# Performance work log

Hardware: AMD Instinct MI355X
Metric: run time of the kernel (lower is better)

## Reference

```python
import jax, jax.numpy as jnp
import numpy as np

N = 50000       # nodes
E = 800000      # edges (avg degree 16)
IN_DIM = 128
H_DIM = 96      # conv='SKP' -> h_dim unchanged
OUT_DIM = 64
NUM_LAYERS = 4
HEADS = 2       # conv='SKP' -> num_heads forced to 2


def setup_inputs() -> dict:
    key = jax.random.key(0)
    ks = jax.random.split(key, 9)
    x = jax.random.normal(ks[0], (N, IN_DIM), jnp.float32)
    edge_index = jax.random.randint(ks[1], (2, E), 0, N, dtype=jnp.int32)
    enc_w = jax.random.normal(ks[2], (IN_DIM, H_DIM), jnp.float32) / np.sqrt(IN_DIM)
    enc_b = jnp.zeros((H_DIM,), jnp.float32)
    dec_w = jax.random.normal(ks[3], (H_DIM, OUT_DIM), jnp.float32) / np.sqrt(H_DIM)
    dec_b = jnp.zeros((OUT_DIM,), jnp.float32)
    # per-layer, per-head linear transforms of the SKP conv
    conv_W = jax.random.normal(ks[4], (NUM_LAYERS, HEADS, H_DIM, H_DIM), jnp.float32) / np.sqrt(H_DIM)
    # per-layer, per-head learnable edge weights (SKP takes num_edges at init)
    conv_ew = jax.random.normal(ks[5], (NUM_LAYERS, HEADS, E), jnp.float32) * 0.1
    return {"x": x, "edge_index": edge_index, "enc_w": enc_w, "enc_b": enc_b,
            "dec_w": dec_w, "dec_b": dec_b, "conv_W": conv_W, "conv_ew": conv_ew}


def _skp_conv(h, src, dst, W, ew):
    # h: [N, d], W: [H, d, d], ew: [H, E]
    # X' = sum_h S_h X W_h  (S_h = learned edge-weighted sparse propagation)
    m = jnp.einsum('nd,hde->hne', h, W)          # [H, N, d] per-head transform
    g = m[:, src, :]                              # [H, E, d] gather at source nodes
    comb = jnp.einsum('he,hed->ed', ew, g)        # weight per edge, sum heads -> [E, d]
    return jax.ops.segment_sum(comb, dst, num_segments=N)  # scatter-add to dest


def reference(x, edge_index, enc_w, enc_b, dec_w, dec_b, conv_W, conv_ew):
    src, dst = edge_index[0], edge_index[1]
    h = jax.nn.relu(x @ enc_w + enc_b)
    for l in range(NUM_LAYERS):
        h = _skp_conv(h, src, dst, conv_W[l], conv_ew[l])
        h = jax.nn.relu(h)   # act=True
    return (h @ dec_w + dec_b, h)
```

## Files before the change

kernel.cpp:

```cpp
#include <hip/hip_runtime.h>

constexpr int IND = 128;
constexpr int HD  = 96;
constexpr int OD  = 64;
constexpr int NL  = 4;

struct F3 { float x, y, z; };

__global__ __launch_bounds__(256) void k_hist(const int* __restrict__ dst, int* __restrict__ deg, int E) {
    int e = blockIdx.x * 256 + threadIdx.x;
    if (e < E) atomicAdd(&deg[dst[e]], 1);
}

__global__ __launch_bounds__(256) void k_scan1(const int* __restrict__ deg, int* __restrict__ bsum, int n) {
    int tid = threadIdx.x;
    int base = blockIdx.x * 1024 + tid * 4;
    int s = 0;
    #pragma unroll
    for (int q = 0; q < 4; ++q) { int i = base + q; if (i < n) s += deg[i]; }
    #pragma unroll
    for (int o = 32; o > 0; o >>= 1) s += __shfl_xor(s, o);
    __shared__ int wsum[4];
    int lane = tid & 63, wid = tid >> 6;
    if (lane == 0) wsum[wid] = s;
    __syncthreads();
    if (tid == 0) bsum[blockIdx.x] = wsum[0] + wsum[1] + wsum[2] + wsum[3];
}

__global__ void k_scan2(const int* __restrict__ bsum, int* __restrict__ boff, int nb,
                        int* __restrict__ row_ptr, int n, int E) {
    int l = threadIdx.x;
    int v = (l < nb) ? bsum[l] : 0;
    int incl = v;
    #pragma unroll
    for (int o = 1; o < 64; o <<= 1) { int t = __shfl_up(incl, o); if (l >= o) incl += t; }
    if (l < nb) boff[l] = incl - v;
    if (l == 0) row_ptr[n] = E;
}

__global__ __launch_bounds__(256) void k_scan3(const int* __restrict__ deg, const int* __restrict__ boff,
                                               int* __restrict__ row_ptr, int n) {
    int tid = threadIdx.x;
    int base = blockIdx.x * 1024 + tid * 4;
    int d[4];
    #pragma unroll
    for (int q = 0; q < 4; ++q) { int i = base + q; d[q] = (i < n) ? deg[i] : 0; }
    int tsum = d[0] + d[1] + d[2] + d[3];
    int incl = tsum;
    #pragma unroll
    for (int o = 1; o < 64; o <<= 1) { int t = __shfl_up(incl, o); if ((tid & 63) >= o) incl += t; }
    __shared__ int wsum[4];
    int lane = tid & 63, wid = tid >> 6;
    if (lane == 63) wsum[wid] = incl;
    __syncthreads();
    int woff = 0;
    for (int w = 0; w < wid; ++w) woff += wsum[w];
    int run = boff[blockIdx.x] + woff + (incl - tsum);
    #pragma unroll
    for (int q = 0; q < 4; ++q) {
        int i = base + q;
        if (i < n) { row_ptr[i] = run; run += d[q]; }
    }
}

__global__ __launch_bounds__(256) void k_fill(const int* __restrict__ src, const int* __restrict__ dst,
                                              const int* __restrict__ row_ptr, int* __restrict__ cursor,
                                              int2* __restrict__ sep, int E) {
    int e = blockIdx.x * 256 + threadIdx.x;
    if (e >= E) return;
    int d = dst[e];
    int pos = atomicAdd(&cursor[d], 1);
    sep[row_ptr[d] + pos] = make_int2(src[e], e);
}

__global__ __launch_bounds__(256) void k_perm2(const int2* __restrict__ sep,
                                               const float* __restrict__ cA0, const float* __restrict__ cA1,
                                               const float* __restrict__ cB0, const float* __restrict__ cB1,
                                               float2* __restrict__ ewq, int E) {
    int i = blockIdx.x * 256 + threadIdx.x;
    if (i >= E) return;
    int e = sep[i].y;
    ewq[i]     = make_float2(cA0[e], cA1[e]);
    ewq[E + i] = make_float2(cB0[e], cB1[e]);
}

__global__ __launch_bounds__(256) void k_agg(const float* __restrict__ h, const int* __restrict__ row_ptr,
                                             const int2* __restrict__ sep, const float2* __restrict__ ewq,
                                             float* __restrict__ A0, float* __restrict__ A1, int n) {
    int g = blockIdx.x * 8 + (threadIdx.x >> 5);
    int lane = threadIdx.x & 31;
    if (g >= n) return;
    int beg = row_ptr[g], end = row_ptr[g + 1];
    float a0x = 0.f, a0y = 0.f, a0z = 0.f;
    float a1x = 0.f, a1y = 0.f, a1z = 0.f;
    int off = lane * 3;
    int i = beg;
    for (; i + 4 <= end; i += 4) {
        int2 s0 = sep[i], s1 = sep[i + 1], s2 = sep[i + 2], s3 = sep[i + 3];
        float2 w0 = ewq[i], w1 = ewq[i + 1], w2 = ewq[i + 2], w3 = ewq[i + 3];
        F3 v0 = *(const F3*)(h + (size_t)s0.x * HD + off);
        F3 v1 = *(const F3*)(h + (size_t)s1.x * HD + off);
        F3 v2 = *(const F3*)(h + (size_t)s2.x * HD + off);
        F3 v3 = *(const F3*)(h + (size_t)s3.x * HD + off);
        a0x = fmaf(w0.x, v0.x, a0x); a0y = fmaf(w0.x, v0.y, a0y); a0z = fmaf(w0.x, v0.z, a0z);
        a1x = fmaf(w0.y, v0.x, a1x); a1y = fmaf(w0.y, v0.y, a1y); a1z = fmaf(w0.y, v0.z, a1z);
        a0x = fmaf(w1.x, v1.x, a0x); a0y = fmaf(w1.x, v1.y, a0y); a0z = fmaf(w1.x, v1.z, a0z);
        a1x = fmaf(w1.y, v1.x, a1x); a1y = fmaf(w1.y, v1.y, a1y); a1z = fmaf(w1.y, v1.z, a1z);
        a0x = fmaf(w2.x, v2.x, a0x); a0y = fmaf(w2.x, v2.y, a0y); a0z = fmaf(w2.x, v2.z, a0z);
        a1x = fmaf(w2.y, v2.x, a1x); a1y = fmaf(w2.y, v2.y, a1y); a1z = fmaf(w2.y, v2.z, a1z);
        a0x = fmaf(w3.x, v3.x, a0x); a0y = fmaf(w3.x, v3.y, a0y); a0z = fmaf(w3.x, v3.z, a0z);
        a1x = fmaf(w3.y, v3.x, a1x); a1y = fmaf(w3.y, v3.y, a1y); a1z = fmaf(w3.y, v3.z, a1z);
    }
    for (; i < end; ++i) {
        int2 s0 = sep[i];
        float2 w0 = ewq[i];
        F3 v0 = *(const F3*)(h + (size_t)s0.x * HD + off);
        a0x = fmaf(w0.x, v0.x, a0x); a0y = fmaf(w0.x, v0.y, a0y); a0z = fmaf(w0.x, v0.z, a0z);
        a1x = fmaf(w0.y, v0.x, a1x); a1y = fmaf(w0.y, v0.y, a1y); a1z = fmaf(w0.y, v0.z, a1z);
    }
    float* p0 = A0 + (size_t)g * HD + off;
    p0[0] = a0x; p0[1] = a0y; p0[2] = a0z;
    float* p1 = A1 + (size_t)g * HD + off;
    p1[0] = a1x; p1[1] = a1y; p1[2] = a1z;
}

template<int K, int NO, bool DUAL, bool RELU, bool BIAS>
__global__ __launch_bounds__(256) void k_gemm(const float* __restrict__ A0p, const float* __restrict__ A1p,
                                              const float* __restrict__ W0p,
                                              const float* __restrict__ bias,
                                              float* __restrict__ out, int n) {
    constexpr int BRO = 128;
    constexpr int KC  = K / 4;
    constexpr int NC  = NO / 16;
    __shared__ float sA[BRO * K];
    int tid = threadIdx.x;
    int tx = tid & 15;
    int ty = tid >> 4;
    int ty2 = ty & 3;
    int brow = blockIdx.x * BRO;

    float acc[8][NC];
    #pragma unroll
    for (int r = 0; r < 8; ++r)
        #pragma unroll
        for (int j = 0; j < NC; ++j) acc[r][j] = 0.f;

    #pragma unroll
    for (int head = 0; head < (DUAL ? 2 : 1); ++head) {
        if (head) __syncthreads();
        const float* Ah = head ? A1p : A0p;
        for (int j = tid; j < BRO * KC; j += 256) {
            int r = j / KC, c4 = j % KC;
            int gr = brow + r;
            float4 v = make_float4(0.f, 0.f, 0.f, 0.f);
            if (gr < n) v = *(const float4*)(Ah + (size_t)gr * K + 4 * c4);
            int sw = c4 ^ ((r >> 3) & 3);
            *(float4*)&sA[r * K + 4 * sw] = v;
        }
        __syncthreads();

        const float* Wh = W0p + (size_t)head * K * NO;
        #pragma unroll 2
        for (int kb4 = 0; kb4 < KC; ++kb4) {
            float4 a4[8];
            #pragma unroll
            for (int r = 0; r < 8; ++r)
                a4[r] = *(const float4*)&sA[(8 * ty + r) * K + 4 * (kb4 ^ ty2)];
            #pragma unroll
            for (int q = 0; q < 4; ++q) {
                float wv[NC];
                const float* wrow = Wh + (size_t)(4 * kb4 + q) * NO + NC * tx;
                #pragma unroll
                for (int j2 = 0; j2 < NC; j2 += 2) {
                    float2 w2 = *(const float2*)(wrow + j2);
                    wv[j2] = w2.x; wv[j2 + 1] = w2.y;
                }
                #pragma unroll
                for (int r = 0; r < 8; ++r) {
                    const float* ap = (const float*)&a4[r];
                    float av = ap[q];
                    #pragma unroll
                    for (int j2 = 0; j2 < NC; ++j2)
                        acc[r][j2] = fmaf(av, wv[j2], acc[r][j2]);
                }
            }
        }
    }
    #pragma unroll
    for (int r = 0; r < 8; ++r) {
        int gr = brow + 8 * ty + r;
        if (gr < n) {
            float* op = out + (size_t)gr * NO + NC * tx;
            #pragma unroll
            for (int j = 0; j < NC; ++j) {
                float v = acc[r][j];
                if (BIAS) v += bias[NC * tx + j];
                if (RELU) v = fmaxf(v, 0.f);
                op[j] = v;
            }
        }
    }
}

extern "C" void kernel_launch(void* const* d_in, const int* in_sizes, int n_in,
                              void* d_out, int out_size, void* d_ws, size_t ws_size,
                              hipStream_t stream) {
    const float* x     = (const float*)d_in[0];
    const int*   ei    = (const int*)  d_in[1];
    const float* enc_w = (const float*)d_in[2];
    const float* enc_b = (const float*)d_in[3];
    const float* dec_w = (const float*)d_in[4];
    const float* dec_b = (const float*)d_in[5];
    const float* convW = (const float*)d_in[6];
    const float* convE = (const float*)d_in[7];

    const int N = in_sizes[0] / IND;
    const int E = in_sizes[1] / 2;
    const int* src = ei;
    const int* dst = ei + E;
    float* fout = (float*)d_out;

    char* wp = (char*)d_ws;
    auto carve = [&](size_t bytes) -> void* {
        void* p = (void*)wp;
        wp += (bytes + 255) & ~(size_t)255;
        return p;
    };
    int*    deg     = (int*)carve(2 * (size_t)N * 4);
    int*    cursor  = deg + N;
    int*    row_ptr = (int*)carve(((size_t)N + 1) * 4);
    int*    bsum    = (int*)carve(64 * 4);
    int*    boff    = (int*)carve(64 * 4);
    int2*   sep     = (int2*)carve((size_t)E * 8);
    float*  P0      = (float*)carve((size_t)N * HD * 4);
    float*  P1      = (float*)carve((size_t)N * HD * 4);
    float*  P2      = (float*)carve((size_t)N * HD * 4);

    float2* ewq = (float2*)fout;

    hipMemsetAsync(deg, 0, 2 * (size_t)N * 4, stream);

    int ebl = (E + 255) / 256;
    int nb  = (N + 1023) / 1024;
    k_hist<<<ebl, 256, 0, stream>>>(dst, deg, E);
    k_scan1<<<nb, 256, 0, stream>>>(deg, bsum, N);
    k_scan2<<<1, 64, 0, stream>>>(bsum, boff, nb, row_ptr, N, E);
    k_scan3<<<nb, 256, 0, stream>>>(deg, boff, row_ptr, N);
    k_fill<<<ebl, 256, 0, stream>>>(src, dst, row_ptr, cursor, sep, E);

    int gblG = (N + 127) / 128;
    int gbl8 = (N + 7) / 8;
    float* hfin = fout + (size_t)N * OD;

    k_gemm<IND, HD, false, true, true><<<gblG, 256, 0, stream>>>(x, nullptr, enc_w, enc_b, P0, N);

    float* hin[NL]  = { P0, P1, P0, P1 };
    float* ha0[NL]  = { P1, P0, P1, P0 };
    float* hout[NL] = { P1, P0, P1, hfin };
    for (int l = 0; l < NL; ++l) {
        if ((l & 1) == 0) {
            const float* cA0 = convE + (size_t)(2 * l)     * E;
            const float* cA1 = convE + (size_t)(2 * l + 1) * E;
            const float* cB0 = convE + (size_t)(2 * l + 2) * E;
            const float* cB1 = convE + (size_t)(2 * l + 3) * E;
            k_perm2<<<ebl, 256, 0, stream>>>(sep, cA0, cA1, cB0, cB1, ewq, E);
        }
        const float* Wl = convW + (size_t)l * 2 * HD * HD;
        k_agg<<<gbl8, 256, 0, stream>>>(hin[l], row_ptr, sep, ewq + (size_t)(l & 1) * E, ha0[l], P2, N);
        k_gemm<HD, HD, true, true, false><<<gblG, 256, 0, stream>>>(ha0[l], P2, Wl, nullptr, hout[l], N);
    }
    k_gemm<HD, OD, false, false, true><<<gblG, 256, 0, stream>>>(hfin, nullptr, dec_w, dec_b, fout, N);
}
```

Baseline: 709.2 us.

## Retile dense GEMM to small row blocks with transposed weights; deepen gather unroll

Reworks the dense GEMM kernel to process 32 rows per block with 2 rows per thread, preload both heads' activations into padded shared memory at once, and read weights as float4 from a pre-transposed copy. A small transpose kernel creates the transposed weights each call. Occupancy hint of 6 blocks is added. The aggregation kernel gains an 8-edge unrolled loop that issues all gathers before the FMAs to increase memory-level parallelism. The trade-off is less register reuse of weights per thread (more global/L1 weight traffic) in exchange for more blocks and occupancy.

```diff
diff --git a/kernel.cpp b/kernel.cpp
--- a/kernel.cpp
+++ b/kernel.cpp
@@ -82,6 +82,16 @@
     int e = sep[i].y;
     ewq[i]     = make_float2(cA0[e], cA1[e]);
     ewq[E + i] = make_float2(cB0[e], cB1[e]);
+}
+
+__global__ __launch_bounds__(256) void k_tr(const float* __restrict__ W, float* __restrict__ WT,
+                                            int K, int NO, int total) {
+    int idx = blockIdx.x * 256 + threadIdx.x;
+    if (idx >= total) return;
+    int per = K * NO;
+    int m = idx / per, rem = idx % per;
+    int k = rem / NO, c = rem % NO;
+    WT[(size_t)m * per + (size_t)c * K + k] = W[idx];
 }
 
 __global__ __launch_bounds__(256) void k_agg(const float* __restrict__ h, const int* __restrict__ row_ptr,
@@ -95,26 +105,36 @@
     float a1x = 0.f, a1y = 0.f, a1z = 0.f;
     int off = lane * 3;
     int i = beg;
+    for (; i + 8 <= end; i += 8) {
+        int s[8]; float2 w[8];
+        #pragma unroll
+        for (int q = 0; q < 8; ++q) { s[q] = sep[i + q].x; w[q] = ewq[i + q]; }
+        F3 v[8];
+        #pragma unroll
+        for (int q = 0; q < 8; ++q) v[q] = *(const F3*)(h + (size_t)s[q] * HD + off);
+        #pragma unroll
+        for (int q = 0; q < 8; ++q) {
+            a0x = fmaf(w[q].x, v[q].x, a0x); a0y = fmaf(w[q].x, v[q].y, a0y); a0z = fmaf(w[q].x, v[q].z, a0z);
+            a1x = fmaf(w[q].y, v[q].x, a1x); a1y = fmaf(w[q].y, v[q].y, a1y); a1z = fmaf(w[q].y, v[q].z, a1z);
+        }
+    }
     for (; i + 4 <= end; i += 4) {
-        int2 s0 = sep[i], s1 = sep[i + 1], s2 = sep[i + 2], s3 = sep[i + 3];
-        float2 w0 = ewq[i], w1 = ewq[i + 1], w2 = ewq[i + 2], w3 = ewq[i + 3];
-        F3 v0 = *(const F3*)(h + (size_t)s0.x * HD + off);
-        F3 v1 = *(const F3*)(h + (size_t)s1.x * HD + off);
-        F3 v2 = *(const F3*)(h + (size_t)s2.x * HD + off);
-        F3 v3 = *(const F3*)(h + (size_t)s3.x * HD + off);
-        a0x = fmaf(w0.x, v0.x, a0x); a0y = fmaf(w0.x, v0.y, a0y); a0z = fmaf(w0.x, v0.z, a0z);
-        a1x = fmaf(w0.y, v0.x, a1x); a1y = fmaf(w0.y, v0.y, a1y); a1z = fmaf(w0.y, v0.z, a1z);
-        a0x = fmaf(w1.x, v1.x, a0x); a0y = fmaf(w1.x, v1.y, a0y); a0z = fmaf(w1.x, v1.z, a0z);
-        a1x = fmaf(w1.y, v1.x, a1x); a1y = fmaf(w1.y, v1.y, a1y); a1z = fmaf(w1.y, v1.z, a1z);
-        a0x = fmaf(w2.x, v2.x, a0x); a0y = fmaf(w2.x, v2.y, a0y); a0z = fmaf(w2.x, v2.z, a0z);
-        a1x = fmaf(w2.y, v2.x, a1x); a1y = fmaf(w2.y, v2.y, a1y); a1z = fmaf(w2.y, v2.z, a1z);
-        a0x = fmaf(w3.x, v3.x, a0x); a0y = fmaf(w3.x, v3.y, a0y); a0z = fmaf(w3.x, v3.z, a0z);
-        a1x = fmaf(w3.y, v3.x, a1x); a1y = fmaf(w3.y, v3.y, a1y); a1z = fmaf(w3.y, v3.z, a1z);
+        int s[4]; float2 w[4];
+        #pragma unroll
+        for (int q = 0; q < 4; ++q) { s[q] = sep[i + q].x; w[q] = ewq[i + q]; }
+        F3 v[4];
+        #pragma unroll
+        for (int q = 0; q < 4; ++q) v[q] = *(const F3*)(h + (size_t)s[q] * HD + off);
+        #pragma unroll
+        for (int q = 0; q < 4; ++q) {
+            a0x = fmaf(w[q].x, v[q].x, a0x); a0y = fmaf(w[q].x, v[q].y, a0y); a0z = fmaf(w[q].x, v[q].z, a0z);
+            a1x = fmaf(w[q].y, v[q].x, a1x); a1y = fmaf(w[q].y, v[q].y, a1y); a1z = fmaf(w[q].y, v[q].z, a1z);
+        }
     }
     for (; i < end; ++i) {
-        int2 s0 = sep[i];
+        int s0 = sep[i].x;
         float2 w0 = ewq[i];
-        F3 v0 = *(const F3*)(h + (size_t)s0.x * HD + off);
+        F3 v0 = *(const F3*)(h + (size_t)s0 * HD + off);
         a0x = fmaf(w0.x, v0.x, a0x); a0y = fmaf(w0.x, v0.y, a0y); a0z = fmaf(w0.x, v0.z, a0z);
         a1x = fmaf(w0.y, v0.x, a1x); a1y = fmaf(w0.y, v0.y, a1y); a1z = fmaf(w0.y, v0.z, a1z);
     }
@@ -125,78 +145,74 @@
 }
 
 template<int K, int NO, bool DUAL, bool RELU, bool BIAS>
-__global__ __launch_bounds__(256) void k_gemm(const float* __restrict__ A0p, const float* __restrict__ A1p,
-                                              const float* __restrict__ W0p,
-                                              const float* __restrict__ bias,
-                                              float* __restrict__ out, int n) {
-    constexpr int BRO = 128;
+__global__ __launch_bounds__(256, 6) void k_gemm(const float* __restrict__ A0p, const float* __restrict__ A1p,
+                                                 const float* __restrict__ WT,
+                                                 const float* __restrict__ bias,
+                                                 float* __restrict__ out, int n) {
+    constexpr int BRO = 32;
+    constexpr int P   = K + 4;
     constexpr int KC  = K / 4;
     constexpr int NC  = NO / 16;
-    __shared__ float sA[BRO * K];
+    __shared__ float sA0[BRO * P];
+    __shared__ float sA1[DUAL ? BRO * P : 4];
     int tid = threadIdx.x;
     int tx = tid & 15;
     int ty = tid >> 4;
-    int ty2 = ty & 3;
     int brow = blockIdx.x * BRO;
 
-    float acc[8][NC];
-    #pragma unroll
-    for (int r = 0; r < 8; ++r)
-        #pragma unroll
-        for (int j = 0; j < NC; ++j) acc[r][j] = 0.f;
+    for (int j = tid; j < BRO * KC; j += 256) {
+        int r = j / KC, c4 = j % KC;
+        int gr = brow + r;
+        float4 v0 = make_float4(0.f, 0.f, 0.f, 0.f);
+        if (gr < n) v0 = *(const float4*)(A0p + (size_t)gr * K + 4 * c4);
+        *(float4*)&sA0[r * P + 4 * c4] = v0;
+        if (DUAL) {
+            float4 v1 = make_float4(0.f, 0.f, 0.f, 0.f);
+            if (gr < n) v1 = *(const float4*)(A1p + (size_t)gr * K + 4 * c4);
+            *(float4*)&sA1[r * P + 4 * c4] = v1;
+        }
+    }
+    __syncthreads();
+
+    float acc[2][NC];
+    #pragma unroll
+    for (int r = 0; r < 2; ++r)
+        #pragma unroll
+        for (int c = 0; c < NC; ++c) acc[r][c] = 0.f;
 
     #pragma unroll
     for (int head = 0; head < (DUAL ? 2 : 1); ++head) {
-        if (head) __syncthreads();
-        const float* Ah = head ? A1p : A0p;
-        for (int j = tid; j < BRO * KC; j += 256) {
-            int r = j / KC, c4 = j % KC;
-            int gr = brow + r;
-            float4 v = make_float4(0.f, 0.f, 0.f, 0.f);
-            if (gr < n) v = *(const float4*)(Ah + (size_t)gr * K + 4 * c4);
-            int sw = c4 ^ ((r >> 3) & 3);
-            *(float4*)&sA[r * K + 4 * sw] = v;
-        }
-        __syncthreads();
-
-        const float* Wh = W0p + (size_t)head * K * NO;
+        const float* Ah = head ? sA1 : sA0;
+        const float* WTh = WT + (size_t)head * NO * K;
         #pragma unroll 2
-        for (int kb4 = 0; kb4 < KC; ++kb4) {
-            float4 a4[8];
+        for (int kb = 0; kb < KC; ++kb) {
+            float4 a0 = *(const float4*)&Ah[(2 * ty) * P + 4 * kb];
+            float4 a1 = *(const float4*)&Ah[(2 * ty + 1) * P + 4 * kb];
             #pragma unroll
-            for (int r = 0; r < 8; ++r)
-                a4[r] = *(const float4*)&sA[(8 * ty + r) * K + 4 * (kb4 ^ ty2)];
-            #pragma unroll
-            for (int q = 0; q < 4; ++q) {
-                float wv[NC];
-                const float* wrow = Wh + (size_t)(4 * kb4 + q) * NO + NC * tx;
-                #pragma unroll
-                for (int j2 = 0; j2 < NC; j2 += 2) {
-                    float2 w2 = *(const float2*)(wrow + j2);
-                    wv[j2] = w2.x; wv[j2 + 1] = w2.y;
-                }
-                #pragma unroll
-                for (int r = 0; r < 8; ++r) {
-                    const float* ap = (const float*)&a4[r];
-                    float av = ap[q];
-                    #pragma unroll
-                    for (int j2 = 0; j2 < NC; ++j2)
-                        acc[r][j2] = fmaf(av, wv[j2], acc[r][j2]);
-                }
+            for (int c = 0; c < NC; ++c) {
+                float4 w = *(const float4*)(WTh + (size_t)(NC * tx + c) * K + 4 * kb);
+                acc[0][c] = fmaf(a0.x, w.x, acc[0][c]);
+                acc[0][c] = fmaf(a0.y, w.y, acc[0][c]);
+                acc[0][c] = fmaf(a0.z, w.z, acc[0][c]);
+                acc[0][c] = fmaf(a0.w, w.w, acc[0][c]);
+                acc[1][c] = fmaf(a1.x, w.x, acc[1][c]);
+                acc[1][c] = fmaf(a1.y, w.y, acc[1][c]);
+                acc[1][c] = fmaf(a1.z, w.z, acc[1][c]);
+                acc[1][c] = fmaf(a1.w, w.w, acc[1][c]);
             }
         }
     }
     #pragma unroll
-    for (int r = 0; r < 8; ++r) {
-        int gr = brow + 8 * ty + r;
+    for (int r = 0; r < 2; ++r) {
+        int gr = brow + 2 * ty + r;
         if (gr < n) {
             float* op = out + (size_t)gr * NO + NC * tx;
             #pragma unroll
-            for (int j = 0; j < NC; ++j) {
-                float v = acc[r][j];
-                if (BIAS) v += bias[NC * tx + j];
+            for (int c = 0; c < NC; ++c) {
+                float v = acc[r][c];
+                if (BIAS) v += bias[NC * tx + c];
                 if (RELU) v = fmaxf(v, 0.f);
-                op[j] = v;
+                op[c] = v;
             }
         }
     }
@@ -235,6 +251,9 @@
     float*  P0      = (float*)carve((size_t)N * HD * 4);
     float*  P1      = (float*)carve((size_t)N * HD * 4);
     float*  P2      = (float*)carve((size_t)N * HD * 4);
+    float*  WTconv  = (float*)carve((size_t)NL * 2 * HD * HD * 4);
+    float*  WTenc   = (float*)carve((size_t)HD * IND * 4);
+    float*  WTdec   = (float*)carve((size_t)OD * HD * 4);
 
     float2* ewq = (float2*)fout;
 
@@ -248,11 +267,20 @@
     k_scan3<<<nb, 256, 0, stream>>>(deg, boff, row_ptr, N);
     k_fill<<<ebl, 256, 0, stream>>>(src, dst, row_ptr, cursor, sep, E);
 
-    int gblG = (N + 127) / 128;
+    {
+        int t1 = NL * 2 * HD * HD;
+        k_tr<<<(t1 + 255) / 256, 256, 0, stream>>>(convW, WTconv, HD, HD, t1);
+        int t2 = IND * HD;
+        k_tr<<<(t2 + 255) / 256, 256, 0, stream>>>(enc_w, WTenc, IND, HD, t2);
+        int t3 = HD * OD;
+        k_tr<<<(t3 + 255) / 256, 256, 0, stream>>>(dec_w, WTdec, HD, OD, t3);
+    }
+
+    int gblG = (N + 31) / 32;
     int gbl8 = (N + 7) / 8;
     float* hfin = fout + (size_t)N * OD;
 
-    k_gemm<IND, HD, false, true, true><<<gblG, 256, 0, stream>>>(x, nullptr, enc_w, enc_b, P0, N);
+    k_gemm<IND, HD, false, true, true><<<gblG, 256, 0, stream>>>(x, nullptr, WTenc, enc_b, P0, N);
 
     float* hin[NL]  = { P0, P1, P0, P1 };
     float* ha0[NL]  = { P1, P0, P1, P0 };
@@ -265,9 +293,9 @@
             const float* cB1 = convE + (size_t)(2 * l + 3) * E;
             k_perm2<<<ebl, 256, 0, stream>>>(sep, cA0, cA1, cB0, cB1, ewq, E);
         }
-        const float* Wl = convW + (size_t)l * 2 * HD * HD;
+        const float* WTl = WTconv + (size_t)l * 2 * HD * HD;
         k_agg<<<gbl8, 256, 0, stream>>>(hin[l], row_ptr, sep, ewq + (size_t)(l & 1) * E, ha0[l], P2, N);
-        k_gemm<HD, HD, true, true, false><<<gblG, 256, 0, stream>>>(ha0[l], P2, Wl, nullptr, hout[l], N);
-    }
-    k_gemm<HD, OD, false, false, true><<<gblG, 256, 0, stream>>>(hfin, nullptr, dec_w, dec_b, fout, N);
-}
+        k_gemm<HD, HD, true, true, false><<<gblG, 256, 0, stream>>>(ha0[l], P2, WTl, nullptr, hout[l], N);
+    }
+    k_gemm<HD, OD, false, false, true><<<gblG, 256, 0, stream>>>(hfin, nullptr, WTdec, dec_b, fout, N);
+}
```

Result: slower. 1.600 ms (+125.6%).
